# Performance work log

Hardware: AMD Instinct MI355X
Metric: run time of the kernel (lower is better)

Reference implementation:

```python
import jax, jax.numpy as jnp
import numpy as np

N_NODES = 50000


def gcn_conv(x, W, b, src, dst, n_nodes):
    # PyG GCNConv: h = D^{-1/2} (A + I) D^{-1/2} (x W) + b
    h = x @ W  # [N, out]
    # degree with self loops: deg[i] = in_degree(i) + 1
    deg = jax.ops.segment_sum(jnp.ones_like(dst, dtype=h.dtype), dst, num_segments=n_nodes) + 1.0
    dis = jax.lax.rsqrt(deg)  # deg >= 1 always
    norm = dis[src] * dis[dst]  # [E]
    # gather-scale-scatter over edges
    agg = jax.ops.segment_sum(h[src] * norm[:, None], dst, num_segments=n_nodes)
    # self-loop contribution: norm_ii = dis[i]^2
    agg = agg + h * (dis * dis)[:, None]
    return agg + b


def setup_inputs() -> dict:
    key = jax.random.key(0)
    k1, k2, k3, k4, k5, k6 = jax.random.split(key, 6)
    latent, hidden, out = 64, 96, 64
    x = jax.random.normal(k1, (N_NODES, latent), dtype=jnp.float32)
    edge_index = jax.random.randint(k2, (2, 800000), 0, N_NODES, dtype=jnp.int64)
    W1 = jax.random.normal(k3, (latent, hidden), dtype=jnp.float32) / np.sqrt(latent)
    b1 = jnp.zeros((hidden,), dtype=jnp.float32)
    W2 = jax.random.normal(k4, (hidden, out), dtype=jnp.float32) / np.sqrt(hidden)
    b2 = jnp.zeros((out,), dtype=jnp.float32)
    return {"x": x, "edge_index": edge_index, "W1": W1, "b1": b1, "W2": W2, "b2": b2}


def reference(x, edge_index, W1, b1, W2, b2):
    src, dst = edge_index[0], edge_index[1]
    n = x.shape[0]
    h = jax.nn.relu(gcn_conv(x, W1, b1, src, dst, n))
    out = jax.nn.sigmoid(gcn_conv(h, W2, b2, src, dst, n))
    return out
```

## Files before the change

### kernel.cpp

```cpp
#include <hip/hip_runtime.h>
#include <hip/hip_bf16.h>
#include <hip/hip_fp16.h>

constexpr int G1 = 96;
constexpr int RNODES = 12544;
constexpr int CAP = 64;

__global__ __launch_bounds__(256) void histo_kernel(const int* __restrict__ dst,
                                                    unsigned short* __restrict__ hist,
                                                    int E, int chunk, int npad2) {
    __shared__ unsigned int h32[RNODES / 2];
    int g = blockIdx.x;
    int base = blockIdx.y * RNODES;
    int e0 = g * chunk;
    int e1 = min(e0 + chunk, E);
    for (int i = threadIdx.x; i < RNODES / 2; i += 256) h32[i] = 0;
    __syncthreads();
    for (int e = e0 + threadIdx.x; e < e1; e += 256) {
        int d = dst[e] - base;
        if (d >= 0 && d < RNODES) atomicAdd(&h32[d >> 1], 1u << ((d & 1) * 16));
    }
    __syncthreads();
    for (int i = threadIdx.x; i < RNODES; i += 256) {
        unsigned int v = (h32[i >> 1] >> ((i & 1) * 16)) & 0xFFFFu;
        hist[(size_t)g * npad2 + base + i] = (unsigned short)v;
    }
}

__global__ __launch_bounds__(256) void colscan_cast_kernel(
    const unsigned short* __restrict__ hist, unsigned short* __restrict__ off16,
    int* __restrict__ cnt, float* __restrict__ dis, const float* __restrict__ x,
    __half* __restrict__ Th, int N, int npad2) {
    __shared__ float sdis[256];
    int n0 = blockIdx.x * 256;
    int d = n0 + threadIdx.x;
    float dv = 0.f;
    if (d < N) {
        int run = 0;
        for (int g = 0; g < G1; ++g) {
            off16[(size_t)g * npad2 + d] = (unsigned short)run;
            run += hist[(size_t)g * npad2 + d];
        }
        cnt[d] = run;
        dv = rsqrtf((float)run + 1.0f);
        dis[d] = dv;
    }
    sdis[threadIdx.x] = dv;
    __syncthreads();
    int total = min(256, N - n0) * 64;
    size_t base_elem = (size_t)n0 * 64;
    for (int l = threadIdx.x * 8; l < total; l += 256 * 8) {
        float dn = sdis[l >> 6];
        float4 a = *(const float4*)(x + base_elem + l);
        float4 b = *(const float4*)(x + base_elem + l + 4);
        __half2 h[4];
        h[0] = __floats2half2_rn(a.x * dn, a.y * dn);
        h[1] = __floats2half2_rn(a.z * dn, a.w * dn);
        h[2] = __floats2half2_rn(b.x * dn, b.y * dn);
        h[3] = __floats2half2_rn(b.z * dn, b.w * dn);
        *(float4*)(Th + base_elem + l) = *(float4*)h;
    }
}

__global__ __launch_bounds__(256) void fill_bucket16_kernel(
    const int* __restrict__ src, const int* __restrict__ dst,
    const unsigned short* __restrict__ off16, unsigned short* __restrict__ csr16,
    int E, int chunk, int npad2) {
    __shared__ unsigned int c16[RNODES / 2];
    int g = blockIdx.x;
    int base = blockIdx.y * RNODES;
    const unsigned int* op = (const unsigned int*)(off16 + (size_t)g * npad2 + base);
    for (int i = threadIdx.x; i < RNODES / 2; i += 256) c16[i] = op[i];
    __syncthreads();
    int e0 = g * chunk;
    int e1 = min(e0 + chunk, E);
    for (int e = e0 + threadIdx.x; e < e1; e += 256) {
        int d = dst[e] - base;
        if (d >= 0 && d < RNODES) {
            unsigned int sh = (d & 1) * 16;
            unsigned int old = atomicAdd(&c16[d >> 1], 1u << sh);
            unsigned int rank = (old >> sh) & 0xFFFFu;
            if (rank < CAP) csr16[(size_t)(base + d) * CAP + rank] = (unsigned short)src[e];
        }
    }
}

__global__ void zero_int_kernel(int* __restrict__ p, int N) {
    int i = blockIdx.x * blockDim.x + threadIdx.x;
    if (i < N) p[i] = 0;
}
__global__ void degree_int_kernel(const int* __restrict__ dst, int* __restrict__ cnt, int E) {
    int i = blockIdx.x * blockDim.x + threadIdx.x;
    if (i < E) atomicAdd(&cnt[dst[i]], 1);
}
__global__ void dis_from_cnt_kernel(const int* __restrict__ cnt, float* __restrict__ dis, int N) {
    int i = blockIdx.x * blockDim.x + threadIdx.x;
    if (i < N) dis[i] = rsqrtf((float)cnt[i] + 1.0f);
}
__global__ __launch_bounds__(1024) void scan_kernel(const int* __restrict__ cnt,
                                                    int* __restrict__ cursor, int N) {
    constexpr int T = 1024;
    __shared__ int sums[T];
    int t = threadIdx.x;
    int ch = (N + T - 1) / T;
    int base = t * ch;
    int local = 0;
    for (int k = 0; k < ch; ++k) {
        int idx = base + k;
        if (idx < N) local += cnt[idx];
    }
    sums[t] = local;
    __syncthreads();
    for (int off = 1; off < T; off <<= 1) {
        int add = (t >= off) ? sums[t - off] : 0;
        __syncthreads();
        sums[t] += add;
        __syncthreads();
    }
    int run = sums[t] - local;
    for (int k = 0; k < ch; ++k) {
        int idx = base + k;
        if (idx < N) {
            cursor[idx] = run;
            run += cnt[idx];
        }
    }
}
__global__ void fill_atomic_kernel(const int* __restrict__ src, const int* __restrict__ dst,
                                   int* __restrict__ cursor_mut, int* __restrict__ csr_src,
                                   int E) {
    int e = blockIdx.x * blockDim.x + threadIdx.x;
    if (e >= E) return;
    int pos = atomicAdd(&cursor_mut[dst[e]], 1);
    csr_src[pos] = src[e];
}
__global__ void cast_scale_kernel(const float* __restrict__ X, const float* __restrict__ dis,
                                  __half* __restrict__ Th, int N) {
    int i = blockIdx.x * blockDim.x + threadIdx.x;
    int n = i >> 3;
    if (n >= N) return;
    int c = (i & 7) * 8;
    float dn = dis[n];
    float4 a = *(const float4*)(X + (size_t)n * 64 + c);
    float4 b = *(const float4*)(X + (size_t)n * 64 + c + 4);
    __half2 h[4];
    h[0] = __floats2half2_rn(a.x * dn, a.y * dn);
    h[1] = __floats2half2_rn(a.z * dn, a.w * dn);
    h[2] = __floats2half2_rn(b.x * dn, b.y * dn);
    h[3] = __floats2half2_rn(b.z * dn, b.w * dn);
    *(float4*)(Th + (size_t)n * 64 + c) = *(float4*)h;
}

template <int CAPT, typename IDX>
__global__ __launch_bounds__(256) void agg0_kernel(const int* __restrict__ cursor,
                                                   const int* __restrict__ cnt,
                                                   const IDX* __restrict__ csr,
                                                   const float* __restrict__ dis,
                                                   const __half* __restrict__ Xh,
                                                   __half* __restrict__ Yh, int N) {
    int i = blockIdx.x * 256 + threadIdx.x;
    int n = i >> 2;
    if (n >= N) return;
    int c = (i & 3) * 16;
    int beg = CAPT ? n * CAPT : cursor[n];
    int cn = cnt[n];
    int end = beg + (CAPT ? min(cn, CAPT) : cn);
    float a[16] = {};
    for (int j = beg; j < end; ++j) {
        int s = (int)csr[j];
        const __half* row = Xh + (size_t)s * 64 + c;
        float4 r0 = *(const float4*)(row);
        float4 r1 = *(const float4*)(row + 8);
        const __half2* h0 = (const __half2*)&r0;
        const __half2* h1 = (const __half2*)&r1;
#pragma unroll
        for (int q = 0; q < 4; ++q) {
            float2 f0 = __half22float2(h0[q]);
            float2 f1 = __half22float2(h1[q]);
            a[2 * q] += f0.x;
            a[2 * q + 1] += f0.y;
            a[8 + 2 * q] += f1.x;
            a[8 + 2 * q + 1] += f1.y;
        }
    }
    {
        const __half* row = Xh + (size_t)n * 64 + c;
        float4 r0 = *(const float4*)(row);
        float4 r1 = *(const float4*)(row + 8);
        const __half2* h0 = (const __half2*)&r0;
        const __half2* h1 = (const __half2*)&r1;
#pragma unroll
        for (int q = 0; q < 4; ++q) {
            float2 f0 = __half22float2(h0[q]);
            float2 f1 = __half22float2(h1[q]);
            a[2 * q] += f0.x;
            a[2 * q + 1] += f0.y;
            a[8 + 2 * q] += f1.x;
            a[8 + 2 * q + 1] += f1.y;
        }
    }
    float dn = dis[n];
    __half2 o[8];
#pragma unroll
    for (int q = 0; q < 8; ++q)
        o[q] = __floats2half2_rn(a[2 * q] * dn, a[2 * q + 1] * dn);
    __half* yp = Yh + (size_t)n * 64 + c;
    *(float4*)(yp) = ((float4*)o)[0];
    *(float4*)(yp + 8) = ((float4*)o)[1];
}

__global__ __launch_bounds__(256) void gemm12_kernel(const __half* __restrict__ Yh,
                                                     const float* __restrict__ W1,
                                                     const float* __restrict__ b1,
                                                     const float* __restrict__ W2,
                                                     const float* __restrict__ dis,
                                                     __half* __restrict__ Th2, int N) {
    constexpr int XS = 100;
    __shared__ float Xs[64 * XS];
    __shared__ float Ws[6144];
    const int n0 = blockIdx.x * 64;
    const int t = threadIdx.x;
    const int tn = t >> 4;
    const int tf = t & 15;

    for (int i = t; i < 6144 / 4; i += 256)
        ((float4*)Ws)[i] = ((const float4*)W1)[i];
    for (int i = t; i < 512; i += 256) {
        int row = i >> 3;
        int c8 = (i & 7) * 8;
        float4 raw = make_float4(0.f, 0.f, 0.f, 0.f);
        if (n0 + row < N) raw = *(const float4*)(Yh + (size_t)(n0 + row) * 64 + c8);
        const __half2* hp = (const __half2*)&raw;
        float* p = Xs + row * XS + c8;
#pragma unroll
        for (int q = 0; q < 4; ++q) {
            float2 f = __half22float2(hp[q]);
            p[2 * q] = f.x;
            p[2 * q + 1] = f.y;
        }
    }
    float breg[6];
#pragma unroll
    for (int j = 0; j < 6; ++j) breg[j] = b1[tf * 6 + j];
    __syncthreads();

    float h[4][6] = {};
    for (int k0 = 0; k0 < 64; k0 += 4) {
        float4 xv[4];
#pragma unroll
        for (int i = 0; i < 4; ++i) xv[i] = *(const float4*)(Xs + (tn * 4 + i) * XS + k0);
        float wv[4][6];
#pragma unroll
        for (int j4 = 0; j4 < 4; ++j4)
#pragma unroll
            for (int j = 0; j < 3; ++j) {
                float2 w2 = *(const float2*)(Ws + (k0 + j4) * 96 + tf * 6 + 2 * j);
                wv[j4][2 * j] = w2.x;
                wv[j4][2 * j + 1] = w2.y;
            }
#pragma unroll
        for (int i = 0; i < 4; ++i) {
            const float xk[4] = {xv[i].x, xv[i].y, xv[i].z, xv[i].w};
#pragma unroll
            for (int j4 = 0; j4 < 4; ++j4)
#pragma unroll
                for (int j = 0; j < 6; ++j) h[i][j] += xk[j4] * wv[j4][j];
        }
    }
#pragma unroll
    for (int i = 0; i < 4; ++i)
#pragma unroll
        for (int j = 0; j < 6; ++j) h[i][j] = fmaxf(h[i][j] + breg[j], 0.f);
    __syncthreads();

#pragma unroll
    for (int i = 0; i < 4; ++i)
#pragma unroll
        for (int j = 0; j < 6; ++j) Xs[(tn * 4 + i) * XS + tf * 6 + j] = h[i][j];
    for (int i = t; i < 6144 / 4; i += 256)
        ((float4*)Ws)[i] = ((const float4*)W2)[i];
    __syncthreads();

    float acc[4][4] = {};
    for (int k0 = 0; k0 < 96; k0 += 4) {
        float4 xv[4];
#pragma unroll
        for (int i = 0; i < 4; ++i) xv[i] = *(const float4*)(Xs + (tn * 4 + i) * XS + k0);
        float wv[4][4];
#pragma unroll
        for (int j4 = 0; j4 < 4; ++j4)
#pragma unroll
            for (int j = 0; j < 2; ++j) {
                float2 w2 = *(const float2*)(Ws + (k0 + j4) * 64 + tf * 4 + 2 * j);
                wv[j4][2 * j] = w2.x;
                wv[j4][2 * j + 1] = w2.y;
            }
#pragma unroll
        for (int i = 0; i < 4; ++i) {
            const float xk[4] = {xv[i].x, xv[i].y, xv[i].z, xv[i].w};
#pragma unroll
            for (int j4 = 0; j4 < 4; ++j4)
#pragma unroll
                for (int j = 0; j < 4; ++j) acc[i][j] += xk[j4] * wv[j4][j];
        }
    }
#pragma unroll
    for (int i = 0; i < 4; ++i) {
        int n = n0 + tn * 4 + i;
        if (n < N) {
            float dn = dis[n];
            __half* op = Th2 + (size_t)n * 64 + tf * 4;
            *(__half2*)(op) = __floats2half2_rn(acc[i][0] * dn, acc[i][1] * dn);
            *(__half2*)(op + 2) = __floats2half2_rn(acc[i][2] * dn, acc[i][3] * dn);
        }
    }
}

template <int CAPT, typename IDX>
__global__ __launch_bounds__(256) void agg1_kernel(const int* __restrict__ cursor,
                                                   const int* __restrict__ cnt,
                                                   const IDX* __restrict__ csr,
                                                   const float* __restrict__ dis,
                                                   const __half* __restrict__ Xh,
                                                   const float* __restrict__ b,
                                                   float* __restrict__ out, int N) {
    int i = blockIdx.x * 256 + threadIdx.x;
    int n = i >> 2;
    if (n >= N) return;
    int c = (i & 3) * 16;
    int beg = CAPT ? n * CAPT : cursor[n];
    int cn = cnt[n];
    int end = beg + (CAPT ? min(cn, CAPT) : cn);
    float a[16] = {};
    for (int j = beg; j < end; ++j) {
        int s = (int)csr[j];
        const __half* row = Xh + (size_t)s * 64 + c;
        float4 r0 = *(const float4*)(row);
        float4 r1 = *(const float4*)(row + 8);
        const __half2* h0 = (const __half2*)&r0;
        const __half2* h1 = (const __half2*)&r1;
#pragma unroll
        for (int q = 0; q < 4; ++q) {
            float2 f0 = __half22float2(h0[q]);
            float2 f1 = __half22float2(h1[q]);
            a[2 * q] += f0.x;
            a[2 * q + 1] += f0.y;
            a[8 + 2 * q] += f1.x;
            a[8 + 2 * q + 1] += f1.y;
        }
    }
    {
        const __half* row = Xh + (size_t)n * 64 + c;
        float4 r0 = *(const float4*)(row);
        float4 r1 = *(const float4*)(row + 8);
        const __half2* h0 = (const __half2*)&r0;
        const __half2* h1 = (const __half2*)&r1;
#pragma unroll
        for (int q = 0; q < 4; ++q) {
            float2 f0 = __half22float2(h0[q]);
            float2 f1 = __half22float2(h1[q]);
            a[2 * q] += f0.x;
            a[2 * q + 1] += f0.y;
            a[8 + 2 * q] += f1.x;
            a[8 + 2 * q + 1] += f1.y;
        }
    }
    float dn = dis[n];
    float r[16];
#pragma unroll
    for (int q = 0; q < 16; ++q) r[q] = 1.f / (1.f + expf(-(a[q] * dn + b[c + q])));
    float* op = out + (size_t)n * 64 + c;
    *(float4*)(op) = make_float4(r[0], r[1], r[2], r[3]);
    *(float4*)(op + 4) = make_float4(r[4], r[5], r[6], r[7]);
    *(float4*)(op + 8) = make_float4(r[8], r[9], r[10], r[11]);
    *(float4*)(op + 12) = make_float4(r[12], r[13], r[14], r[15]);
}

extern "C" void kernel_launch(void* const* d_in, const int* in_sizes, int n_in,
                              void* d_out, int out_size, void* d_ws, size_t ws_size,
                              hipStream_t stream) {
    const float* x  = (const float*)d_in[0];
    const int*   ei = (const int*)d_in[1];
    const float* W1 = (const float*)d_in[2];
    const float* b1 = (const float*)d_in[3];
    const float* W2 = (const float*)d_in[4];
    const float* b2 = (const float*)d_in[5];

    constexpr int LAT = 64;
    const int E = in_sizes[1] / 2;
    const int N = in_sizes[0] / LAT;
    const int* src = ei;
    const int* dst = ei + E;

    const int B = 256;
    auto blocks = [](long total, int b) { return (int)((total + b - 1) / b); };

    const int ranges = (N + RNODES - 1) / RNODES;
    const int npad2 = ranges * RNODES;
    const int chunk = (E + G1 - 1) / G1;

    long nmax = (npad2 > N) ? npad2 : N;
    size_t Na = (size_t)((nmax + 1023) / 1024) * 1024;
    size_t Epad = (size_t)((E + 3) / 4) * 4;
    size_t csrBytes = (size_t)Na * CAP * 2;
    if (csrBytes < Epad * 4) csrBytes = Epad * 4;
    csrBytes = (csrBytes + 15) / 16 * 16;

    int* cnt      = (int*)d_ws;
    int* cursor   = cnt + Na;
    int* cursmut  = cursor + Na;
    float* dis    = (float*)(cursmut + Na);
    char* csr_raw = (char*)(dis + Na);
    unsigned short* csr16 = (unsigned short*)csr_raw;
    int*            csr32 = (int*)csr_raw;
    unsigned short* hist  = (unsigned short*)(csr_raw + csrBytes);
    unsigned short* off16 = hist + (size_t)G1 * npad2;
    __half* Th  = (__half*)(off16 + (size_t)G1 * npad2);
    __half* Th2 = Th + Na * 64;
    __half* Yh  = Th2 + Na * 64;

    size_t need = (char*)(Yh + Na * 64) - (char*)d_ws;
    bool fast = (ws_size >= need) && (chunk < 65536) && (ranges <= 8) && (N <= 65535);

    if (fast) {
        dim3 g2(G1, ranges);
        histo_kernel<<<g2, 256, 0, stream>>>(dst, hist, E, chunk, npad2);
        colscan_cast_kernel<<<blocks(N, 256), 256, 0, stream>>>(hist, off16, cnt, dis, x, Th,
                                                                N, npad2);
        fill_bucket16_kernel<<<g2, 256, 0, stream>>>(src, dst, off16, csr16, E, chunk, npad2);
        agg0_kernel<CAP, unsigned short>
            <<<blocks((long)N * 4, B), B, 0, stream>>>(nullptr, cnt, csr16, dis, Th, Yh, N);
        gemm12_kernel<<<blocks(N, 64), 256, 0, stream>>>(Yh, W1, b1, W2, dis, Th2, N);
        agg1_kernel<CAP, unsigned short>
            <<<blocks((long)N * 4, B), B, 0, stream>>>(nullptr, cnt, csr16, dis, Th2, b2,
                                                       (float*)d_out, N);
    } else {
        zero_int_kernel<<<blocks(N, B), B, 0, stream>>>(cnt, N);
        degree_int_kernel<<<blocks(E, B), B, 0, stream>>>(dst, cnt, E);
        dis_from_cnt_kernel<<<blocks(N, B), B, 0, stream>>>(cnt, dis, N);
        scan_kernel<<<1, 1024, 0, stream>>>(cnt, cursor, N);
        hipMemcpyAsync(cursmut, cursor, (size_t)N * sizeof(int), hipMemcpyDeviceToDevice, stream);
        fill_atomic_kernel<<<blocks(E, B), B, 0, stream>>>(src, dst, cursmut, csr32, E);
        cast_scale_kernel<<<blocks((long)N * 8, B), B, 0, stream>>>(x, dis, Th, N);
        agg0_kernel<0, int>
            <<<blocks((long)N * 4, B), B, 0, stream>>>(cursor, cnt, csr32, dis, Th, Yh, N);
        gemm12_kernel<<<blocks(N, 64), 256, 0, stream>>>(Yh, W1, b1, W2, dis, Th2, N);
        agg1_kernel<0, int>
            <<<blocks((long)N * 4, B), B, 0, stream>>>(cursor, cnt, csr32, dis, Th2, b2,
                                                       (float*)d_out, N);
    }
}
```

Baseline: 198.9 us.

## Fuse CSR build phases into one cooperative kernel with grid syncs

Merges the histogram, column-scan/cast, and bucket-fill kernels into a single cooperative launch that separates the phases with grid-wide syncs. The destination range per block is halved so that twice as many blocks (96 x ranges) fill the grid, and the fast-path limit on ranges rises to 16. The aim is to remove two kernel launches and the gaps between them. In exchange, each block now scans the edge chunk more times because there are more ranges, the kernel pays grid-sync overhead, and every block must be co-resident for the cooperative launch to succeed.

New measurement: 470.7 us. 2.37x slower.

```diff
diff --git a/kernel.cpp b/kernel.cpp
--- a/kernel.cpp
+++ b/kernel.cpp
@@ -1,10 +1,90 @@
 #include <hip/hip_runtime.h>
 #include <hip/hip_bf16.h>
 #include <hip/hip_fp16.h>
+#include <hip/hip_cooperative_groups.h>
+
+namespace cg = cooperative_groups;
 
 constexpr int G1 = 96;
-constexpr int RNODES = 12544;
+constexpr int RNODES = 6272;
 constexpr int CAP = 64;
+
+__global__ __launch_bounds__(256) void build_coop_kernel(
+    const int* __restrict__ src, const int* __restrict__ dst,
+    unsigned short* __restrict__ hist, unsigned short* __restrict__ off16,
+    int* __restrict__ cnt, float* __restrict__ dis, const float* __restrict__ x,
+    __half* __restrict__ Th, unsigned short* __restrict__ csr16,
+    int E, int chunk, int npad2, int N) {
+    cg::grid_group grid = cg::this_grid();
+    __shared__ unsigned int lds[RNODES / 2];
+    __shared__ float sdis[256];
+    const int g = blockIdx.x;
+    const int base = blockIdx.y * RNODES;
+    const int e0 = g * chunk;
+    const int e1 = min(e0 + chunk, E);
+
+    for (int i = threadIdx.x; i < RNODES / 2; i += 256) lds[i] = 0;
+    __syncthreads();
+    for (int e = e0 + threadIdx.x; e < e1; e += 256) {
+        int d = dst[e] - base;
+        if ((unsigned)d < (unsigned)RNODES) atomicAdd(&lds[d >> 1], 1u << ((d & 1) * 16));
+    }
+    __syncthreads();
+    for (int i = threadIdx.x; i < RNODES; i += 256)
+        hist[(size_t)g * npad2 + base + i] =
+            (unsigned short)((lds[i >> 1] >> ((i & 1) * 16)) & 0xFFFFu);
+    __threadfence();
+    grid.sync();
+
+    int bid = blockIdx.y * gridDim.x + blockIdx.x;
+    if (bid * 256 < N) {
+        int d = bid * 256 + threadIdx.x;
+        float dv = 0.f;
+        if (d < N) {
+            int run = 0;
+            for (int gg = 0; gg < G1; ++gg) {
+                off16[(size_t)gg * npad2 + d] = (unsigned short)run;
+                run += hist[(size_t)gg * npad2 + d];
+            }
+            cnt[d] = run;
+            dv = rsqrtf((float)run + 1.0f);
+            dis[d] = dv;
+        }
+        sdis[threadIdx.x] = dv;
+        __syncthreads();
+        int n0 = bid * 256;
+        int total = min(256, N - n0) * 64;
+        size_t be = (size_t)n0 * 64;
+        for (int l = threadIdx.x * 8; l < total; l += 256 * 8) {
+            float dn = sdis[l >> 6];
+            float4 a = *(const float4*)(x + be + l);
+            float4 b = *(const float4*)(x + be + l + 4);
+            __half2 h[4];
+            h[0] = __floats2half2_rn(a.x * dn, a.y * dn);
+            h[1] = __floats2half2_rn(a.z * dn, a.w * dn);
+            h[2] = __floats2half2_rn(b.x * dn, b.y * dn);
+            h[3] = __floats2half2_rn(b.z * dn, b.w * dn);
+            *(float4*)(Th + be + l) = *(float4*)h;
+        }
+    }
+    __threadfence();
+    grid.sync();
+
+    {
+        const unsigned int* op = (const unsigned int*)(off16 + (size_t)g * npad2 + base);
+        for (int i = threadIdx.x; i < RNODES / 2; i += 256) lds[i] = op[i];
+        __syncthreads();
+        for (int e = e0 + threadIdx.x; e < e1; e += 256) {
+            int d = dst[e] - base;
+            if ((unsigned)d < (unsigned)RNODES) {
+                unsigned int sh = (d & 1) * 16;
+                unsigned int old = atomicAdd(&lds[d >> 1], 1u << sh);
+                unsigned int rank = (old >> sh) & 0xFFFFu;
+                if (rank < CAP) csr16[(size_t)(base + d) * CAP + rank] = (unsigned short)src[e];
+            }
+        }
+    }
+}
 
 __global__ __launch_bounds__(256) void histo_kernel(const int* __restrict__ dst,
                                                     unsigned short* __restrict__ hist,
@@ -18,13 +98,12 @@
     __syncthreads();
     for (int e = e0 + threadIdx.x; e < e1; e += 256) {
         int d = dst[e] - base;
-        if (d >= 0 && d < RNODES) atomicAdd(&h32[d >> 1], 1u << ((d & 1) * 16));
-    }
-    __syncthreads();
-    for (int i = threadIdx.x; i < RNODES; i += 256) {
-        unsigned int v = (h32[i >> 1] >> ((i & 1) * 16)) & 0xFFFFu;
-        hist[(size_t)g * npad2 + base + i] = (unsigned short)v;
-    }
+        if ((unsigned)d < (unsigned)RNODES) atomicAdd(&h32[d >> 1], 1u << ((d & 1) * 16));
+    }
+    __syncthreads();
+    for (int i = threadIdx.x; i < RNODES; i += 256)
+        hist[(size_t)g * npad2 + base + i] =
+            (unsigned short)((h32[i >> 1] >> ((i & 1) * 16)) & 0xFFFFu);
 }
 
 __global__ __launch_bounds__(256) void colscan_cast_kernel(
@@ -76,7 +155,7 @@
     int e1 = min(e0 + chunk, E);
     for (int e = e0 + threadIdx.x; e < e1; e += 256) {
         int d = dst[e] - base;
-        if (d >= 0 && d < RNODES) {
+        if ((unsigned)d < (unsigned)RNODES) {
             unsigned int sh = (d & 1) * 16;
             unsigned int old = atomicAdd(&c16[d >> 1], 1u << sh);
             unsigned int rank = (old >> sh) & 0xFFFFu;
@@ -420,14 +499,41 @@
     __half* Yh  = Th2 + Na * 64;
 
     size_t need = (char*)(Yh + Na * 64) - (char*)d_ws;
-    bool fast = (ws_size >= need) && (chunk < 65536) && (ranges <= 8) && (N <= 65535);
+    bool fast = (ws_size >= need) && (chunk < 65536) && (ranges <= 16) && (N <= 65535);
+
+    static int coopSupported = -1;
+    if (coopSupported < 0) {
+        int dev = 0, v = 0;
+        hipGetDevice(&dev);
+        if (hipDeviceGetAttribute(&v, hipDeviceAttributeCooperativeLaunch, dev) != hipSuccess)
+            v = 0;
+        coopSupported = v;
+    }
 
     if (fast) {
         dim3 g2(G1, ranges);
-        histo_kernel<<<g2, 256, 0, stream>>>(dst, hist, E, chunk, npad2);
-        colscan_cast_kernel<<<blocks(N, 256), 256, 0, stream>>>(hist, off16, cnt, dis, x, Th,
-                                                                N, npad2);
-        fill_bucket16_kernel<<<g2, 256, 0, stream>>>(src, dst, off16, csr16, E, chunk, npad2);
+        if (coopSupported) {
+            const int* srcp = src;
+            const int* dstp = dst;
+            unsigned short* histp = hist;
+            unsigned short* offp = off16;
+            int* cntp = cnt;
+            float* disp = dis;
+            const float* xp = x;
+            __half* thp = Th;
+            unsigned short* csrp = csr16;
+            int Ep = E, chp = chunk, npp = npad2, Np = N;
+            void* args[] = {&srcp, &dstp, &histp, &offp, &cntp, &disp, &xp,
+                            &thp,  &csrp, &Ep,    &chp,  &npp,  &Np};
+            hipLaunchCooperativeKernel((const void*)build_coop_kernel, g2, dim3(256), args, 0,
+                                       stream);
+        } else {
+            histo_kernel<<<g2, 256, 0, stream>>>(dst, hist, E, chunk, npad2);
+            colscan_cast_kernel<<<blocks(N, 256), 256, 0, stream>>>(hist, off16, cnt, dis, x,
+                                                                    Th, N, npad2);
+            fill_bucket16_kernel<<<g2, 256, 0, stream>>>(src, dst, off16, csr16, E, chunk,
+                                                         npad2);
+        }
         agg0_kernel<CAP, unsigned short>
             <<<blocks((long)N * 4, B), B, 0, stream>>>(nullptr, cnt, csr16, dis, Th, Yh, N);
         gemm12_kernel<<<blocks(N, 64), 256, 0, stream>>>(Yh, W1, b1, W2, dis, Th2, N);
```
